# Optimization experiments

Hardware: AMD Instinct MI355X
Metric: run time of the kernel (lower is better)

## Reference

```python
import jax, jax.numpy as jnp
import numpy as np

V, E, H, NL = 32000, 400, 1152, 3  # vocab, embed, hidden, layers
T, B = 64, 48


def _uniform(key, shape, std):
    return jax.random.uniform(key, shape, jnp.float32, -std, std)


def setup_inputs() -> dict:
    key = jax.random.key(0)
    ks = jax.random.split(key, 18)
    std = 1.0 / np.sqrt(H)
    inp = {
        "x": jax.random.randint(ks[0], (T, B), 0, V),
        "h0": jnp.zeros((NL, B, H), jnp.float32),
        "c0": jnp.zeros((NL, B, H), jnp.float32),
        "emb_W": jax.random.normal(ks[1], (V, E), jnp.float32) * 0.02,
        # layer 0: input E -> 4H ; layers 1,2: H -> 4H
        "W_i0": _uniform(ks[2], (4 * H, E), std), "b_i0": _uniform(ks[3], (4 * H,), std),
        "W_h0": _uniform(ks[4], (4 * H, H), std), "b_h0": _uniform(ks[5], (4 * H,), std),
        "W_i1": _uniform(ks[6], (4 * H, H), std), "b_i1": _uniform(ks[7], (4 * H,), std),
        "W_h1": _uniform(ks[8], (4 * H, H), std), "b_h1": _uniform(ks[9], (4 * H,), std),
        "W_i2": _uniform(ks[10], (4 * H, H), std), "b_i2": _uniform(ks[11], (4 * H,), std),
        "W_h2": _uniform(ks[12], (4 * H, H), std), "b_h2": _uniform(ks[13], (4 * H,), std),
        "W_dec": _uniform(ks[14], (V, H), 1.0 / np.sqrt(H)),
        "b_dec": _uniform(ks[15], (V,), 1.0 / np.sqrt(H)),
    }
    return inp


def _cell(z, h, c, Wi, bi, Wh, bh):
    # preact: [B, 4H]; gate layout per the original: i | f | o | g
    p = z @ Wi.T + bi + h @ Wh.T + bh
    i = jax.nn.sigmoid(p[:, :H])
    f = jax.nn.sigmoid(p[:, H:2 * H])
    o = jax.nn.sigmoid(p[:, 2 * H:3 * H])
    g = jnp.tanh(p[:, 3 * H:])
    c_t = f * c + i * g
    h_t = o * jnp.tanh(c_t)
    return h_t, c_t


def reference(x, h0, c0, emb_W,
              W_i0, b_i0, W_h0, b_h0,
              W_i1, b_i1, W_h1, b_h1,
              W_i2, b_i2, W_h2, b_h2,
              W_dec, b_dec):
    # eval-mode forward: dropout / drop-connect / variational dropout are identity
    emb = emb_W[x]  # [T, B, E]

    def step(carry, xt):
        ha, ca, hb, cb, hc, cc = carry
        ha, ca = _cell(xt, ha, ca, W_i0, b_i0, W_h0, b_h0)
        hb, cb = _cell(ha, hb, cb, W_i1, b_i1, W_h1, b_h1)
        hc, cc = _cell(hb, hc, cc, W_i2, b_i2, W_h2, b_h2)
        return (ha, ca, hb, cb, hc, cc), hc

    carry0 = (h0[0], c0[0], h0[1], c0[1], h0[2], c0[2])
    (ha, ca, hb, cb, hc, cc), out = jax.lax.scan(step, carry0, emb)  # out: [T, B, H]
    decoded = jnp.einsum('tbh,vh->tbv', out, W_dec) + b_dec  # [T, B, V]
    h_fin = jnp.stack([ha, hb, hc])
    c_fin = jnp.stack([ca, cb, cc])
    return decoded, (h_fin, c_fin)
```

## Files before the change

kernel.cpp:

```cpp
#include <hip/hip_runtime.h>

typedef unsigned short u16;
typedef __attribute__((ext_vector_type(8))) short s16x8;
typedef __attribute__((ext_vector_type(4))) float f32x4;

#define T_ 64
#define B_ 48
#define H_ 1152
#define E_ 400
#define EPAD 416
#define V_ 32000
#define FOURH 4608
#define TB_ 3072
#define HB (B_*H_)
#define LSTRIDE (65*HB)
#define RBLK 256

#define OFF_ZPRE  ((size_t)0)
#define OFF_HHI   ((size_t)56623104)
#define OFF_HLO   ((size_t)78188544)
#define OFF_CST   ((size_t)99753984)
#define OFF_ZH    ((size_t)100417536)
#define OFF_ZL    ((size_t)102973440)
#define OFF_P0    ((size_t)105529344)
#define OFF_CTR   ((size_t)116146176)

__device__ __forceinline__ u16 f2bf(float x) {
    unsigned u = __float_as_uint(x);
    u += 0x7fffu + ((u >> 16) & 1u);
    return (u16)(u >> 16);
}
__device__ __forceinline__ float bf2f(u16 h) {
    return __uint_as_float(((unsigned)h) << 16);
}
__device__ __forceinline__ void split8(const float* p, s16x8& hi, s16x8& lo) {
    f32x4 a = *(const f32x4*)(p);
    f32x4 b = *(const f32x4*)(p + 4);
    float v[8];
#pragma unroll
    for (int j = 0; j < 4; ++j) { v[j] = a[j]; v[j + 4] = b[j]; }
#pragma unroll
    for (int j = 0; j < 8; ++j) {
        u16 h = f2bf(v[j]);
        hi[j] = (short)h;
        lo[j] = (short)f2bf(v[j] - bf2f(h));
    }
}
__device__ __forceinline__ void split8r(f32x4 a, f32x4 b, s16x8& hi, s16x8& lo) {
    float v[8];
#pragma unroll
    for (int j = 0; j < 4; ++j) { v[j] = a[j]; v[j + 4] = b[j]; }
#pragma unroll
    for (int j = 0; j < 8; ++j) {
        u16 h = f2bf(v[j]);
        hi[j] = (short)h;
        lo[j] = (short)f2bf(v[j] - bf2f(h));
    }
}
__device__ __forceinline__ f32x4 mfma16(s16x8 a, s16x8 b, f32x4 c) {
    return __builtin_amdgcn_mfma_f32_16x16x32_bf16(a, b, c, 0, 0, 0);
}

__device__ __forceinline__ float ld_sc(const float* p) {
    return __hip_atomic_load(p, __ATOMIC_RELAXED, __HIP_MEMORY_SCOPE_AGENT);
}
__device__ __forceinline__ void st_sc(float* p, float v) {
    __hip_atomic_store(p, v, __ATOMIC_RELAXED, __HIP_MEMORY_SCOPE_AGENT);
}
__device__ __forceinline__ void st_sc16(u16* p, u16 v) {
    __hip_atomic_store(p, v, __ATOMIC_RELAXED, __HIP_MEMORY_SCOPE_AGENT);
}

__device__ __forceinline__ void grid_barrier(int* ctrs, int nblk) {
    asm volatile("s_waitcnt vmcnt(0)" ::: "memory");
    __syncthreads();
    if (threadIdx.x == 0) {
        int* gen = ctrs + 252;
        int* root = ctrs + 248;
        int* gcnt = ctrs + ((blockIdx.x & 15) << 4);
        const int gsz = nblk >> 4;
        int g = __hip_atomic_load(gen, __ATOMIC_RELAXED, __HIP_MEMORY_SCOPE_AGENT);
        int old = __hip_atomic_fetch_add(gcnt, 1, __ATOMIC_RELAXED, __HIP_MEMORY_SCOPE_AGENT);
        if (old == gsz - 1) {
            __hip_atomic_store(gcnt, 0, __ATOMIC_RELAXED, __HIP_MEMORY_SCOPE_AGENT);
            asm volatile("s_waitcnt vmcnt(0)" ::: "memory");
            int r = __hip_atomic_fetch_add(root, 1, __ATOMIC_RELAXED, __HIP_MEMORY_SCOPE_AGENT);
            if (r == 15) {
                __hip_atomic_store(root, 0, __ATOMIC_RELAXED, __HIP_MEMORY_SCOPE_AGENT);
                asm volatile("s_waitcnt vmcnt(0)" ::: "memory");
                __hip_atomic_fetch_add(gen, 1, __ATOMIC_RELAXED, __HIP_MEMORY_SCOPE_AGENT);
            }
        }
        while (__hip_atomic_load(gen, __ATOMIC_RELAXED, __HIP_MEMORY_SCOPE_AGENT) == g) {
            __builtin_amdgcn_s_sleep(2);
        }
    }
    __syncthreads();
}

__global__ void gather_split_kernel(const int* __restrict__ x, const float* __restrict__ embW,
                                    u16* __restrict__ Zh, u16* __restrict__ Zl) {
    int i = blockIdx.x * blockDim.x + threadIdx.x;
    const int total = TB_ * EPAD;
    if (i >= total) return;
    int tb = i / EPAD, k = i - tb * EPAD;
    float v = 0.f;
    if (k < E_) v = embW[(size_t)x[tb] * E_ + k];
    u16 h = f2bf(v);
    Zh[i] = h;
    Zl[i] = f2bf(v - bf2f(h));
}

__global__ void init_state_kernel(const float* __restrict__ h0, const float* __restrict__ c0,
                                  u16* __restrict__ Hhi, u16* __restrict__ Hlo,
                                  float* __restrict__ Cst) {
    int i = blockIdx.x * blockDim.x + threadIdx.x;
    if (i >= 3 * HB) return;
    int l = i / HB, r = i - l * HB;
    float h = h0[i];
    u16 hh = f2bf(h);
    size_t idx = (size_t)l * LSTRIDE + r;
    Hhi[idx] = hh;
    Hlo[idx] = f2bf(h - bf2f(hh));
    Cst[i] = c0[i];
}

__global__ __launch_bounds__(256, 2) void gemm_bias_kernel(
    const u16* __restrict__ Ahi, const u16* __restrict__ Alo, int lda,
    const float* __restrict__ W, int ldw, int kvalid, int ksteps,
    const float* __restrict__ bias1, const float* __restrict__ bias2,
    float* __restrict__ C, int ldc) {
    const int lane = threadIdx.x & 63;
    const int wv = threadIdx.x >> 6;
    const int m16 = lane & 15, q = lane >> 4;
    const int mbase = blockIdx.y * 192 + wv * 48;
    const int nbase = blockIdx.x * 128;

    f32x4 acc[8][3];
#pragma unroll
    for (int s8 = 0; s8 < 8; ++s8)
#pragma unroll
        for (int mt = 0; mt < 3; ++mt) acc[s8][mt] = (f32x4){0.f, 0.f, 0.f, 0.f};

    const u16* arow[3];
    const u16* alrow[3];
#pragma unroll
    for (int mt = 0; mt < 3; ++mt) {
        size_t m = (size_t)(mbase + mt * 16 + m16);
        arow[mt] = Ahi + m * lda + q * 8;
        alrow[mt] = Alo + m * lda + q * 8;
    }
    const float* wrow[8];
#pragma unroll
    for (int s8 = 0; s8 < 8; ++s8) {
        size_t n = (size_t)(nbase + s8 * 16 + m16);
        wrow[s8] = W + n * ldw + q * 8;
    }

    for (int ks = 0; ks < ksteps; ++ks) {
        int k = ks * 32;
        s16x8 ah[3], al[3];
#pragma unroll
        for (int mt = 0; mt < 3; ++mt) {
            ah[mt] = *(const s16x8*)(arow[mt] + k);
            al[mt] = *(const s16x8*)(alrow[mt] + k);
        }
        int kk = k + q * 8;
#pragma unroll
        for (int s8 = 0; s8 < 8; ++s8) {
            s16x8 wh, wl;
            if (kk + 8 <= kvalid) {
                split8(wrow[s8] + k, wh, wl);
            } else {
#pragma unroll
                for (int j = 0; j < 8; ++j) { wh[j] = 0; wl[j] = 0; }
            }
#pragma unroll
            for (int mt = 0; mt < 3; ++mt) {
                acc[s8][mt] = mfma16(ah[mt], wh, acc[s8][mt]);
                acc[s8][mt] = mfma16(ah[mt], wl, acc[s8][mt]);
                acc[s8][mt] = mfma16(al[mt], wh, acc[s8][mt]);
            }
        }
    }
#pragma unroll
    for (int s8 = 0; s8 < 8; ++s8) {
        int n = nbase + s8 * 16 + m16;
        float bv = (bias1 ? bias1[n] : 0.f) + (bias2 ? bias2[n] : 0.f);
#pragma unroll
        for (int mt = 0; mt < 3; ++mt)
#pragma unroll
            for (int r = 0; r < 4; ++r) {
                int m = mbase + mt * 16 + q * 4 + r;
                C[(size_t)m * ldc + n] = acc[s8][mt][r] + bv;
            }
    }
}

__global__ __launch_bounds__(256, 2) void recur_layer_kernel(
    const float* __restrict__ W,
    const float* __restrict__ bi, const float* __restrict__ bh,
    const float* __restrict__ Zpre,
    u16* __restrict__ Hhi, u16* __restrict__ Hlo,
    float* __restrict__ Cst,
    float* __restrict__ P0, float* __restrict__ P1,
    int* __restrict__ ctrs,
    float* __restrict__ outh, float* __restrict__ outc) {
    const int lane = threadIdx.x & 63;
    const int slot = threadIdx.x >> 6;
    const int blk = blockIdx.x;
    const int m16 = lane & 15, q = lane >> 4;
    const int xg = blk & 7;
    const int li = ((blk >> 3) << 2) + slot;
    const bool havetask = (li < 72);
    const int strip = (li >> 1) * 8 + xg;
    const int kh = li & 1;
    const int n0 = strip * 16;
    const int koff = kh * 576;
    const float* wrow = W + (size_t)(n0 + m16) * H_ + koff + q * 8;
    float* Pout = kh ? P1 : P0;
    const int gi = blk * 256 + (int)threadIdx.x;
    const int gb = gi / H_, gj = gi - gb * H_;

    for (int t = 0; t < 64; ++t) {
        if (havetask) {
            float zin[3][4];
            if (kh == 0) {
                const float* zp = Zpre + (size_t)(t * B_) * FOURH + n0 + m16;
#pragma unroll
                for (int mt = 0; mt < 3; ++mt)
#pragma unroll
                    for (int r = 0; r < 4; ++r)
                        zin[mt][r] = ld_sc(zp + (size_t)(mt * 16 + q * 4 + r) * FOURH);
            } else {
#pragma unroll
                for (int mt = 0; mt < 3; ++mt)
#pragma unroll
                    for (int r = 0; r < 4; ++r) zin[mt][r] = 0.f;
            }
            f32x4 acc[3];
#pragma unroll
            for (int mt = 0; mt < 3; ++mt) acc[mt] = (f32x4){0.f, 0.f, 0.f, 0.f};
            const u16* arow[3];
            const u16* alrow[3];
#pragma unroll
            for (int mt = 0; mt < 3; ++mt) {
                size_t ro = (size_t)t * HB + (size_t)(mt * 16 + m16) * H_ + koff + q * 8;
                arow[mt] = Hhi + ro;
                alrow[mt] = Hlo + ro;
            }
            f32x4 w0A = *(const f32x4*)(wrow);
            f32x4 w0B = *(const f32x4*)(wrow + 4);
            f32x4 w1A = *(const f32x4*)(wrow + 32);
            f32x4 w1B = *(const f32x4*)(wrow + 36);
            s16x8 ah[3], al[3];
#pragma unroll
            for (int mt = 0; mt < 3; ++mt) {
                ah[mt] = *(const s16x8*)(arow[mt]);
                al[mt] = *(const s16x8*)(alrow[mt]);
            }
#pragma unroll 2
            for (int ks = 0; ks < 18; ++ks) {
                int kp1 = ks + 1; if (kp1 > 17) kp1 = 17;
                int kp2 = ks + 2; if (kp2 > 17) kp2 = 17;
                const int kn1 = kp1 * 32, kn2 = kp2 * 32;
                f32x4 w2A = *(const f32x4*)(wrow + kn2);
                f32x4 w2B = *(const f32x4*)(wrow + kn2 + 4);
                s16x8 nah[3], nal[3];
#pragma unroll
                for (int mt = 0; mt < 3; ++mt) {
                    nah[mt] = *(const s16x8*)(arow[mt] + kn1);
                    nal[mt] = *(const s16x8*)(alrow[mt] + kn1);
                }
                s16x8 wh, wl;
                split8r(w0A, w0B, wh, wl);
#pragma unroll
                for (int mt = 0; mt < 3; ++mt) {
                    acc[mt] = mfma16(ah[mt], wh, acc[mt]);
                    acc[mt] = mfma16(ah[mt], wl, acc[mt]);
                    acc[mt] = mfma16(al[mt], wh, acc[mt]);
                }
                w0A = w1A; w0B = w1B; w1A = w2A; w1B = w2B;
#pragma unroll
                for (int mt = 0; mt < 3; ++mt) { ah[mt] = nah[mt]; al[mt] = nal[mt]; }
            }
            float* pout = Pout + n0 + m16;
#pragma unroll
            for (int mt = 0; mt < 3; ++mt)
#pragma unroll
                for (int r = 0; r < 4; ++r)
                    st_sc(pout + (size_t)(mt * 16 + q * 4 + r) * FOURH,
                          acc[mt][r] + zin[mt][r]);
        }
        grid_barrier(ctrs, RBLK);

        if (gi < HB) {
            const float* p0 = P0 + (size_t)gb * FOURH;
            const float* p1 = P1 + (size_t)gb * FOURH;
            float pi = ld_sc(p0 + gj) + ld_sc(p1 + gj) + bi[gj] + bh[gj];
            float pf = ld_sc(p0 + H_ + gj) + ld_sc(p1 + H_ + gj) + bi[H_ + gj] + bh[H_ + gj];
            float po = ld_sc(p0 + 2 * H_ + gj) + ld_sc(p1 + 2 * H_ + gj) + bi[2 * H_ + gj] + bh[2 * H_ + gj];
            float pg = ld_sc(p0 + 3 * H_ + gj) + ld_sc(p1 + 3 * H_ + gj) + bi[3 * H_ + gj] + bh[3 * H_ + gj];
            float c = ld_sc(Cst + gi);
            float ig = 1.f / (1.f + expf(-pi));
            float fg = 1.f / (1.f + expf(-pf));
            float og = 1.f / (1.f + expf(-po));
            float gg = tanhf(pg);
            float cn = fg * c + ig * gg;
            float hn = og * tanhf(cn);
            st_sc(Cst + gi, cn);
            u16 hh = f2bf(hn);
            size_t hidx = (size_t)(t + 1) * HB + gi;
            st_sc16(Hhi + hidx, hh);
            st_sc16(Hlo + hidx, f2bf(hn - bf2f(hh)));
            if (t == 63) {
                outh[gi] = hn;
                outc[gi] = cn;
            }
        }
        grid_barrier(ctrs, RBLK);
    }
}

extern "C" void kernel_launch(void* const* d_in, const int* in_sizes, int n_in,
                              void* d_out, int out_size, void* d_ws, size_t ws_size,
                              hipStream_t stream) {
    (void)in_sizes; (void)n_in; (void)out_size; (void)ws_size;
    const int* x = (const int*)d_in[0];
    const float* h0 = (const float*)d_in[1];
    const float* c0 = (const float*)d_in[2];
    const float* embW = (const float*)d_in[3];
    const float* Wi0 = (const float*)d_in[4];
    const float* bi0 = (const float*)d_in[5];
    const float* Wh0 = (const float*)d_in[6];
    const float* bh0 = (const float*)d_in[7];
    const float* Wi1 = (const float*)d_in[8];
    const float* bi1 = (const float*)d_in[9];
    const float* Wh1 = (const float*)d_in[10];
    const float* bh1 = (const float*)d_in[11];
    const float* Wi2 = (const float*)d_in[12];
    const float* bi2 = (const float*)d_in[13];
    const float* Wh2 = (const float*)d_in[14];
    const float* bh2 = (const float*)d_in[15];
    const float* Wdec = (const float*)d_in[16];
    const float* bdec = (const float*)d_in[17];

    char* ws = (char*)d_ws;
    float* Zpre = (float*)(ws + OFF_ZPRE);
    u16* Hhi = (u16*)(ws + OFF_HHI);
    u16* Hlo = (u16*)(ws + OFF_HLO);
    float* Cst = (float*)(ws + OFF_CST);
    u16* Zh = (u16*)(ws + OFF_ZH);
    u16* Zl = (u16*)(ws + OFF_ZL);
    float* P0 = (float*)(ws + OFF_P0);
    float* P1 = P0 + (size_t)B_ * FOURH;
    int* ctrs = (int*)(ws + OFF_CTR);

    float* decoded = (float*)d_out;
    float* out_h = decoded + (size_t)TB_ * V_;
    float* out_c = out_h + 3 * (size_t)HB;

    hipMemsetAsync(ctrs, 0, 256 * sizeof(int), stream);
    gather_split_kernel<<<(TB_ * EPAD + 255) / 256, 256, 0, stream>>>(x, embW, Zh, Zl);
    init_state_kernel<<<(3 * HB + 255) / 256, 256, 0, stream>>>(h0, c0, Hhi, Hlo, Cst);

    dim3 gZ(FOURH / 128, TB_ / 192);

    gemm_bias_kernel<<<gZ, 256, 0, stream>>>(Zh, Zl, EPAD, Wi0, E_, E_, (E_ + 31) / 32,
                                             nullptr, nullptr, Zpre, FOURH);
    recur_layer_kernel<<<RBLK, 256, 0, stream>>>(Wh0, bi0, bh0, Zpre, Hhi, Hlo, Cst,
                                                 P0, P1, ctrs, out_h, out_c);

    gemm_bias_kernel<<<gZ, 256, 0, stream>>>(Hhi + HB, Hlo + HB, H_, Wi1, H_, H_, H_ / 32,
                                             nullptr, nullptr, Zpre, FOURH);
    recur_layer_kernel<<<RBLK, 256, 0, stream>>>(Wh1, bi1, bh1, Zpre,
                                                 Hhi + LSTRIDE, Hlo + LSTRIDE, Cst + HB,
                                                 P0, P1, ctrs, out_h + HB, out_c + HB);

    gemm_bias_kernel<<<gZ, 256, 0, stream>>>(Hhi + LSTRIDE + HB, Hlo + LSTRIDE + HB, H_,
                                             Wi2, H_, H_, H_ / 32,
                                             nullptr, nullptr, Zpre, FOURH);
    recur_layer_kernel<<<RBLK, 256, 0, stream>>>(Wh2, bi2, bh2, Zpre,
                                                 Hhi + 2 * LSTRIDE, Hlo + 2 * LSTRIDE,
                                                 Cst + 2 * HB,
                                                 P0, P1, ctrs, out_h + 2 * HB, out_c + 2 * HB);

    dim3 gD(V_ / 128, TB_ / 192);
    gemm_bias_kernel<<<gD, 256, 0, stream>>>(Hhi + (size_t)(2 * 65 + 1) * HB,
                                             Hlo + (size_t)(2 * 65 + 1) * HB, H_,
                                             Wdec, H_, H_, H_ / 32,
                                             bdec, nullptr, decoded, V_);
}
```

Baseline: 8.816 ms.

## Fuse LSTM gate update into recurrent GEMM blocks to halve grid barriers

Each recurrent block now owns a strip of 16 gate columns interleaved so that i,f,o,g for the same hidden unit sit in adjacent lanes. The four waves split K and reduce through LDS, and wave 0 applies the gates in registers while keeping the cell state in registers too. This drops the P0/P1 partial-sum round trip through global memory and the second grid barrier per timestep, and the barrier becomes epoch-based with per-group release flags. The GEMM grid is also remapped so panels are assigned per XCD. The trade-off is that wave 0 carries the serial gate work, and the grid grows to 288 blocks, all of which must be co-resident for the barrier to work.

```diff
diff --git a/kernel.cpp b/kernel.cpp
--- a/kernel.cpp
+++ b/kernel.cpp
@@ -14,15 +14,13 @@
 #define TB_ 3072
 #define HB (B_*H_)
 #define LSTRIDE (65*HB)
-#define RBLK 256
+#define RBLK 288
 
 #define OFF_ZPRE  ((size_t)0)
 #define OFF_HHI   ((size_t)56623104)
 #define OFF_HLO   ((size_t)78188544)
-#define OFF_CST   ((size_t)99753984)
 #define OFF_ZH    ((size_t)100417536)
 #define OFF_ZL    ((size_t)102973440)
-#define OFF_P0    ((size_t)105529344)
 #define OFF_CTR   ((size_t)116146176)
 
 __device__ __forceinline__ u16 f2bf(float x) {
@@ -64,22 +62,20 @@
 __device__ __forceinline__ float ld_sc(const float* p) {
     return __hip_atomic_load(p, __ATOMIC_RELAXED, __HIP_MEMORY_SCOPE_AGENT);
 }
-__device__ __forceinline__ void st_sc(float* p, float v) {
-    __hip_atomic_store(p, v, __ATOMIC_RELAXED, __HIP_MEMORY_SCOPE_AGENT);
-}
 __device__ __forceinline__ void st_sc16(u16* p, u16 v) {
     __hip_atomic_store(p, v, __ATOMIC_RELAXED, __HIP_MEMORY_SCOPE_AGENT);
 }
 
-__device__ __forceinline__ void grid_barrier(int* ctrs, int nblk) {
+__device__ __forceinline__ void grid_barrier2(int* ctrs, int epoch) {
     asm volatile("s_waitcnt vmcnt(0)" ::: "memory");
     __syncthreads();
     if (threadIdx.x == 0) {
-        int* gen = ctrs + 252;
-        int* root = ctrs + 248;
-        int* gcnt = ctrs + ((blockIdx.x & 15) << 4);
-        const int gsz = nblk >> 4;
-        int g = __hip_atomic_load(gen, __ATOMIC_RELAXED, __HIP_MEMORY_SCOPE_AGENT);
+        const int grp = blockIdx.x & 15;
+        int* gcnt = ctrs + grp * 16;
+        int* root = ctrs + 256;
+        int* genr = ctrs + 272;
+        int* ggen = ctrs + 288 + grp * 16;
+        const int gsz = RBLK / 16;
         int old = __hip_atomic_fetch_add(gcnt, 1, __ATOMIC_RELAXED, __HIP_MEMORY_SCOPE_AGENT);
         if (old == gsz - 1) {
             __hip_atomic_store(gcnt, 0, __ATOMIC_RELAXED, __HIP_MEMORY_SCOPE_AGENT);
@@ -88,11 +84,17 @@
             if (r == 15) {
                 __hip_atomic_store(root, 0, __ATOMIC_RELAXED, __HIP_MEMORY_SCOPE_AGENT);
                 asm volatile("s_waitcnt vmcnt(0)" ::: "memory");
-                __hip_atomic_fetch_add(gen, 1, __ATOMIC_RELAXED, __HIP_MEMORY_SCOPE_AGENT);
-            }
-        }
-        while (__hip_atomic_load(gen, __ATOMIC_RELAXED, __HIP_MEMORY_SCOPE_AGENT) == g) {
-            __builtin_amdgcn_s_sleep(2);
+                __hip_atomic_fetch_add(genr, 1, __ATOMIC_RELAXED, __HIP_MEMORY_SCOPE_AGENT);
+            } else {
+                while (__hip_atomic_load(genr, __ATOMIC_RELAXED, __HIP_MEMORY_SCOPE_AGENT) <= epoch) {
+                    __builtin_amdgcn_s_sleep(2);
+                }
+            }
+            __hip_atomic_store(ggen, epoch + 1, __ATOMIC_RELAXED, __HIP_MEMORY_SCOPE_AGENT);
+        } else {
+            while (__hip_atomic_load(ggen, __ATOMIC_RELAXED, __HIP_MEMORY_SCOPE_AGENT) <= epoch) {
+                __builtin_amdgcn_s_sleep(2);
+            }
         }
     }
     __syncthreads();
@@ -111,9 +113,8 @@
     Zl[i] = f2bf(v - bf2f(h));
 }
 
-__global__ void init_state_kernel(const float* __restrict__ h0, const float* __restrict__ c0,
-                                  u16* __restrict__ Hhi, u16* __restrict__ Hlo,
-                                  float* __restrict__ Cst) {
+__global__ void init_state_kernel(const float* __restrict__ h0,
+                                  u16* __restrict__ Hhi, u16* __restrict__ Hlo) {
     int i = blockIdx.x * blockDim.x + threadIdx.x;
     if (i >= 3 * HB) return;
     int l = i / HB, r = i - l * HB;
@@ -122,19 +123,23 @@
     size_t idx = (size_t)l * LSTRIDE + r;
     Hhi[idx] = hh;
     Hlo[idx] = f2bf(h - bf2f(hh));
-    Cst[i] = c0[i];
 }
 
 __global__ __launch_bounds__(256, 2) void gemm_bias_kernel(
     const u16* __restrict__ Ahi, const u16* __restrict__ Alo, int lda,
-    const float* __restrict__ W, int ldw, int kvalid, int ksteps,
-    const float* __restrict__ bias1, const float* __restrict__ bias2,
+    const float* __restrict__ W, int ldw, int kvalid, int ksteps, int npanels,
+    const float* __restrict__ bias1,
     float* __restrict__ C, int ldc) {
+    const int id = blockIdx.x;
+    const int xcd = id & 7, slotb = id >> 3;
+    const int panel = (slotb >> 4) * 8 + xcd;
+    const int ytile = slotb & 15;
+    if (panel >= npanels) return;
     const int lane = threadIdx.x & 63;
     const int wv = threadIdx.x >> 6;
     const int m16 = lane & 15, q = lane >> 4;
-    const int mbase = blockIdx.y * 192 + wv * 48;
-    const int nbase = blockIdx.x * 128;
+    const int mbase = ytile * 192 + wv * 48;
+    const int nbase = panel * 128;
 
     f32x4 acc[8][3];
 #pragma unroll
@@ -186,7 +191,7 @@
 #pragma unroll
     for (int s8 = 0; s8 < 8; ++s8) {
         int n = nbase + s8 * 16 + m16;
-        float bv = (bias1 ? bias1[n] : 0.f) + (bias2 ? bias2[n] : 0.f);
+        float bv = bias1 ? bias1[n] : 0.f;
 #pragma unroll
         for (int mt = 0; mt < 3; ++mt)
 #pragma unroll
@@ -201,124 +206,141 @@
     const float* __restrict__ W,
     const float* __restrict__ bi, const float* __restrict__ bh,
     const float* __restrict__ Zpre,
+    const float* __restrict__ c0l,
     u16* __restrict__ Hhi, u16* __restrict__ Hlo,
-    float* __restrict__ Cst,
-    float* __restrict__ P0, float* __restrict__ P1,
-    int* __restrict__ ctrs,
+    int* __restrict__ ctrs, int ep0,
     float* __restrict__ outh, float* __restrict__ outc) {
+    __shared__ float lred[3][12][64];
     const int lane = threadIdx.x & 63;
-    const int slot = threadIdx.x >> 6;
-    const int blk = blockIdx.x;
+    const int wv = threadIdx.x >> 6;
     const int m16 = lane & 15, q = lane >> 4;
-    const int xg = blk & 7;
-    const int li = ((blk >> 3) << 2) + slot;
-    const bool havetask = (li < 72);
-    const int strip = (li >> 1) * 8 + xg;
-    const int kh = li & 1;
-    const int n0 = strip * 16;
-    const int koff = kh * 576;
-    const float* wrow = W + (size_t)(n0 + m16) * H_ + koff + q * 8;
-    float* Pout = kh ? P1 : P0;
-    const int gi = blk * 256 + (int)threadIdx.x;
-    const int gb = gi / H_, gj = gi - gb * H_;
+    const int g = lane & 3;
+    const int strip = blockIdx.x;
+    const int nprime = strip * 16 + m16;
+    const int j = nprime >> 2;
+    const int n_nat = (nprime & 3) * H_ + j;
+    const int koff = wv * 288;
+
+    float biasn = 0.f;
+    float creg0 = 0.f, creg1 = 0.f, creg2 = 0.f;
+    if (wv == 0) {
+        biasn = bi[n_nat] + bh[n_nat];
+        creg0 = c0l[(0 * 16 + q * 4 + g) * H_ + j];
+        creg1 = c0l[(1 * 16 + q * 4 + g) * H_ + j];
+        creg2 = c0l[(2 * 16 + q * 4 + g) * H_ + j];
+    }
+    const float* wrow = W + (size_t)n_nat * H_ + koff + q * 8;
 
     for (int t = 0; t < 64; ++t) {
-        if (havetask) {
-            float zin[3][4];
-            if (kh == 0) {
-                const float* zp = Zpre + (size_t)(t * B_) * FOURH + n0 + m16;
-#pragma unroll
-                for (int mt = 0; mt < 3; ++mt)
-#pragma unroll
-                    for (int r = 0; r < 4; ++r)
-                        zin[mt][r] = ld_sc(zp + (size_t)(mt * 16 + q * 4 + r) * FOURH);
-            } else {
-#pragma unroll
-                for (int mt = 0; mt < 3; ++mt)
-#pragma unroll
-                    for (int r = 0; r < 4; ++r) zin[mt][r] = 0.f;
-            }
-            f32x4 acc[3];
-#pragma unroll
-            for (int mt = 0; mt < 3; ++mt) acc[mt] = (f32x4){0.f, 0.f, 0.f, 0.f};
-            const u16* arow[3];
-            const u16* alrow[3];
+        float zin[3][4];
+        if (wv == 0) {
+            const float* zp = Zpre + (size_t)(t * B_) * FOURH + n_nat;
+#pragma unroll
+            for (int mt = 0; mt < 3; ++mt)
+#pragma unroll
+                for (int r = 0; r < 4; ++r)
+                    zin[mt][r] = ld_sc(zp + (size_t)(mt * 16 + q * 4 + r) * FOURH);
+        }
+        f32x4 acc[3];
+#pragma unroll
+        for (int mt = 0; mt < 3; ++mt) acc[mt] = (f32x4){0.f, 0.f, 0.f, 0.f};
+        const u16* arow[3];
+        const u16* alrow[3];
+#pragma unroll
+        for (int mt = 0; mt < 3; ++mt) {
+            size_t ro = (size_t)t * HB + (size_t)(mt * 16 + m16) * H_ + koff + q * 8;
+            arow[mt] = Hhi + ro;
+            alrow[mt] = Hlo + ro;
+        }
+        f32x4 w0A = *(const f32x4*)(wrow);
+        f32x4 w0B = *(const f32x4*)(wrow + 4);
+        f32x4 w1A = *(const f32x4*)(wrow + 32);
+        f32x4 w1B = *(const f32x4*)(wrow + 36);
+        s16x8 ah0[3], al0[3], ah1[3], al1[3];
+#pragma unroll
+        for (int mt = 0; mt < 3; ++mt) {
+            ah0[mt] = *(const s16x8*)(arow[mt]);
+            al0[mt] = *(const s16x8*)(alrow[mt]);
+            ah1[mt] = *(const s16x8*)(arow[mt] + 32);
+            al1[mt] = *(const s16x8*)(alrow[mt] + 32);
+        }
+#pragma unroll
+        for (int ks = 0; ks < 9; ++ks) {
+            const int kp2 = (ks + 2 <= 8) ? ks + 2 : 8;
+            const int kn2 = kp2 * 32;
+            f32x4 w2A = *(const f32x4*)(wrow + kn2);
+            f32x4 w2B = *(const f32x4*)(wrow + kn2 + 4);
+            s16x8 ah2[3], al2[3];
 #pragma unroll
             for (int mt = 0; mt < 3; ++mt) {
-                size_t ro = (size_t)t * HB + (size_t)(mt * 16 + m16) * H_ + koff + q * 8;
-                arow[mt] = Hhi + ro;
-                alrow[mt] = Hlo + ro;
-            }
-            f32x4 w0A = *(const f32x4*)(wrow);
-            f32x4 w0B = *(const f32x4*)(wrow + 4);
-            f32x4 w1A = *(const f32x4*)(wrow + 32);
-            f32x4 w1B = *(const f32x4*)(wrow + 36);
-            s16x8 ah[3], al[3];
+                ah2[mt] = *(const s16x8*)(arow[mt] + kn2);
+                al2[mt] = *(const s16x8*)(alrow[mt] + kn2);
+            }
+            s16x8 wh, wl;
+            split8r(w0A, w0B, wh, wl);
 #pragma unroll
             for (int mt = 0; mt < 3; ++mt) {
-                ah[mt] = *(const s16x8*)(arow[mt]);
-                al[mt] = *(const s16x8*)(alrow[mt]);
-            }
-#pragma unroll 2
-            for (int ks = 0; ks < 18; ++ks) {
-                int kp1 = ks + 1; if (kp1 > 17) kp1 = 17;
-                int kp2 = ks + 2; if (kp2 > 17) kp2 = 17;
-                const int kn1 = kp1 * 32, kn2 = kp2 * 32;
-                f32x4 w2A = *(const f32x4*)(wrow + kn2);
-                f32x4 w2B = *(const f32x4*)(wrow + kn2 + 4);
-                s16x8 nah[3], nal[3];
-#pragma unroll
-                for (int mt = 0; mt < 3; ++mt) {
-                    nah[mt] = *(const s16x8*)(arow[mt] + kn1);
-                    nal[mt] = *(const s16x8*)(alrow[mt] + kn1);
+                acc[mt] = mfma16(ah0[mt], wh, acc[mt]);
+                acc[mt] = mfma16(ah0[mt], wl, acc[mt]);
+                acc[mt] = mfma16(al0[mt], wh, acc[mt]);
+            }
+            w0A = w1A; w0B = w1B; w1A = w2A; w1B = w2B;
+#pragma unroll
+            for (int mt = 0; mt < 3; ++mt) {
+                ah0[mt] = ah1[mt]; al0[mt] = al1[mt];
+                ah1[mt] = ah2[mt]; al1[mt] = al2[mt];
+            }
+        }
+        if (wv > 0) {
+#pragma unroll
+            for (int mt = 0; mt < 3; ++mt)
+#pragma unroll
+                for (int r = 0; r < 4; ++r)
+                    lred[wv - 1][mt * 4 + r][lane] = acc[mt][r];
+        }
+        __syncthreads();
+        if (wv == 0) {
+#pragma unroll
+            for (int mt = 0; mt < 3; ++mt)
+#pragma unroll
+                for (int r = 0; r < 4; ++r)
+                    acc[mt][r] += lred[0][mt * 4 + r][lane] + lred[1][mt * 4 + r][lane] +
+                                  lred[2][mt * 4 + r][lane] + zin[mt][r] + biasn;
+#pragma unroll
+            for (int mt = 0; mt < 3; ++mt) {
+#pragma unroll
+                for (int r = 0; r < 4; ++r) {
+                    float y = acc[mt][r];
+                    float y1 = __shfl_xor(y, 1);
+                    float y2 = __shfl_xor(y, 2);
+                    float y3 = __shfl_xor(y, 3);
+                    if (r == g) {
+                        float pi = (g == 0) ? y : (g == 1) ? y1 : (g == 2) ? y2 : y3;
+                        float pf = (g == 0) ? y1 : (g == 1) ? y : (g == 2) ? y3 : y2;
+                        float po = (g == 0) ? y2 : (g == 1) ? y3 : (g == 2) ? y : y1;
+                        float pg_ = (g == 0) ? y3 : (g == 1) ? y2 : (g == 2) ? y1 : y;
+                        float ig = 1.f / (1.f + expf(-pi));
+                        float fg = 1.f / (1.f + expf(-pf));
+                        float og = 1.f / (1.f + expf(-po));
+                        float gg = tanhf(pg_);
+                        float cprev = (mt == 0) ? creg0 : (mt == 1) ? creg1 : creg2;
+                        float cn = fg * cprev + ig * gg;
+                        float hn = og * tanhf(cn);
+                        if (mt == 0) creg0 = cn; else if (mt == 1) creg1 = cn; else creg2 = cn;
+                        u16 hh = f2bf(hn);
+                        int b = mt * 16 + q * 4 + g;
+                        size_t hidx = (size_t)(t + 1) * HB + (size_t)b * H_ + j;
+                        st_sc16(Hhi + hidx, hh);
+                        st_sc16(Hlo + hidx, f2bf(hn - bf2f(hh)));
+                        if (t == 63) {
+                            outh[b * H_ + j] = hn;
+                            outc[b * H_ + j] = cn;
+                        }
+                    }
                 }
-                s16x8 wh, wl;
-                split8r(w0A, w0B, wh, wl);
-#pragma unroll
-                for (int mt = 0; mt < 3; ++mt) {
-                    acc[mt] = mfma16(ah[mt], wh, acc[mt]);
-                    acc[mt] = mfma16(ah[mt], wl, acc[mt]);
-                    acc[mt] = mfma16(al[mt], wh, acc[mt]);
-                }
-                w0A = w1A; w0B = w1B; w1A = w2A; w1B = w2B;
-#pragma unroll
-                for (int mt = 0; mt < 3; ++mt) { ah[mt] = nah[mt]; al[mt] = nal[mt]; }
-            }
-            float* pout = Pout + n0 + m16;
-#pragma unroll
-            for (int mt = 0; mt < 3; ++mt)
-#pragma unroll
-                for (int r = 0; r < 4; ++r)
-                    st_sc(pout + (size_t)(mt * 16 + q * 4 + r) * FOURH,
-                          acc[mt][r] + zin[mt][r]);
-        }
-        grid_barrier(ctrs, RBLK);
-
-        if (gi < HB) {
-            const float* p0 = P0 + (size_t)gb * FOURH;
-            const float* p1 = P1 + (size_t)gb * FOURH;
-            float pi = ld_sc(p0 + gj) + ld_sc(p1 + gj) + bi[gj] + bh[gj];
-            float pf = ld_sc(p0 + H_ + gj) + ld_sc(p1 + H_ + gj) + bi[H_ + gj] + bh[H_ + gj];
-            float po = ld_sc(p0 + 2 * H_ + gj) + ld_sc(p1 + 2 * H_ + gj) + bi[2 * H_ + gj] + bh[2 * H_ + gj];
-            float pg = ld_sc(p0 + 3 * H_ + gj) + ld_sc(p1 + 3 * H_ + gj) + bi[3 * H_ + gj] + bh[3 * H_ + gj];
-            float c = ld_sc(Cst + gi);
-            float ig = 1.f / (1.f + expf(-pi));
-            float fg = 1.f / (1.f + expf(-pf));
-            float og = 1.f / (1.f + expf(-po));
-            float gg = tanhf(pg);
-            float cn = fg * c + ig * gg;
-            float hn = og * tanhf(cn);
-            st_sc(Cst + gi, cn);
-            u16 hh = f2bf(hn);
-            size_t hidx = (size_t)(t + 1) * HB + gi;
-            st_sc16(Hhi + hidx, hh);
-            st_sc16(Hlo + hidx, f2bf(hn - bf2f(hh)));
-            if (t == 63) {
-                outh[gi] = hn;
-                outc[gi] = cn;
-            }
-        }
-        grid_barrier(ctrs, RBLK);
+            }
+        }
+        grid_barrier2(ctrs, ep0 + t);
     }
 }
 
@@ -349,45 +371,39 @@
     float* Zpre = (float*)(ws + OFF_ZPRE);
     u16* Hhi = (u16*)(ws + OFF_HHI);
     u16* Hlo = (u16*)(ws + OFF_HLO);
-    float* Cst = (float*)(ws + OFF_CST);
     u16* Zh = (u16*)(ws + OFF_ZH);
     u16* Zl = (u16*)(ws + OFF_ZL);
-    float* P0 = (float*)(ws + OFF_P0);
-    float* P1 = P0 + (size_t)B_ * FOURH;
     int* ctrs = (int*)(ws + OFF_CTR);
 
     float* decoded = (float*)d_out;
     float* out_h = decoded + (size_t)TB_ * V_;
     float* out_c = out_h + 3 * (size_t)HB;
 
-    hipMemsetAsync(ctrs, 0, 256 * sizeof(int), stream);
+    hipMemsetAsync(ctrs, 0, 4096, stream);
     gather_split_kernel<<<(TB_ * EPAD + 255) / 256, 256, 0, stream>>>(x, embW, Zh, Zl);
-    init_state_kernel<<<(3 * HB + 255) / 256, 256, 0, stream>>>(h0, c0, Hhi, Hlo, Cst);
-
-    dim3 gZ(FOURH / 128, TB_ / 192);
-
-    gemm_bias_kernel<<<gZ, 256, 0, stream>>>(Zh, Zl, EPAD, Wi0, E_, E_, (E_ + 31) / 32,
-                                             nullptr, nullptr, Zpre, FOURH);
-    recur_layer_kernel<<<RBLK, 256, 0, stream>>>(Wh0, bi0, bh0, Zpre, Hhi, Hlo, Cst,
-                                                 P0, P1, ctrs, out_h, out_c);
-
-    gemm_bias_kernel<<<gZ, 256, 0, stream>>>(Hhi + HB, Hlo + HB, H_, Wi1, H_, H_, H_ / 32,
-                                             nullptr, nullptr, Zpre, FOURH);
-    recur_layer_kernel<<<RBLK, 256, 0, stream>>>(Wh1, bi1, bh1, Zpre,
-                                                 Hhi + LSTRIDE, Hlo + LSTRIDE, Cst + HB,
-                                                 P0, P1, ctrs, out_h + HB, out_c + HB);
-
+    init_state_kernel<<<(3 * HB + 255) / 256, 256, 0, stream>>>(h0, Hhi, Hlo);
+
+    const int gZ = 8 * ((36 + 7) / 8) * 16;
+    const int gD = 8 * ((250 + 7) / 8) * 16;
+
+    gemm_bias_kernel<<<gZ, 256, 0, stream>>>(Zh, Zl, EPAD, Wi0, E_, E_, (E_ + 31) / 32, 36,
+                                             nullptr, Zpre, FOURH);
+    recur_layer_kernel<<<RBLK, 256, 0, stream>>>(Wh0, bi0, bh0, Zpre, c0,
+                                                 Hhi, Hlo, ctrs, 0, out_h, out_c);
+    gemm_bias_kernel<<<gZ, 256, 0, stream>>>(Hhi + HB, Hlo + HB, H_, Wi1, H_, H_, H_ / 32, 36,
+                                             nullptr, Zpre, FOURH);
+    recur_layer_kernel<<<RBLK, 256, 0, stream>>>(Wh1, bi1, bh1, Zpre, c0 + HB,
+                                                 Hhi + LSTRIDE, Hlo + LSTRIDE, ctrs, 64,
+                                                 out_h + HB, out_c + HB);
     gemm_bias_kernel<<<gZ, 256, 0, stream>>>(Hhi + LSTRIDE + HB, Hlo + LSTRIDE + HB, H_,
-                                             Wi2, H_, H_, H_ / 32,
-                                             nullptr, nullptr, Zpre, FOURH);
-    recur_layer_kernel<<<RBLK, 256, 0, stream>>>(Wh2, bi2, bh2, Zpre,
-                                                 Hhi + 2 * LSTRIDE, Hlo + 2 * LSTRIDE,
-                                                 Cst + 2 * HB,
-                                                 P0, P1, ctrs, out_h + 2 * HB, out_c + 2 * HB);
-
-    dim3 gD(V_ / 128, TB_ / 192);
+                                             Wi2, H_, H_, H_ / 32, 36,
+                                             nullptr, Zpre, FOURH);
+    recur_layer_kernel<<<RBLK, 256, 0, stream>>>(Wh2, bi2, bh2, Zpre, c0 + 2 * HB,
+                                                 Hhi + 2 * LSTRIDE, Hlo + 2 * LSTRIDE, ctrs, 128,
+                                                 out_h + 2 * HB, out_c + 2 * HB);
+
     gemm_bias_kernel<<<gD, 256, 0, stream>>>(Hhi + (size_t)(2 * 65 + 1) * HB,
                                              Hlo + (size_t)(2 * 65 + 1) * HB, H_,
-                                             Wdec, H_, H_, H_ / 32,
-                                             bdec, nullptr, decoded, V_);
-}
+                                             Wdec, H_, H_, H_ / 32, 250,
+                                             bdec, decoded, V_);
+}
```

Measured after the change: 7.510 ms. 14.8% less time.
